# Kernel tuning notes

Hardware: AMD Instinct MI355X
Metric: run time of the kernel (lower is better)

The kernel has to match this reference:

```python
import jax, jax.numpy as jnp
import numpy as np

N, NB, NP, T = 1024, 16, 256, 80
EPS_LEN = 1e-9   # seg_len clamp_min in original
EPS_DD = 1e-12   # dot(d,d) clamp_min in original


def setup_inputs() -> dict:
    key = jax.random.key(0)
    k1, k2, k3, k4 = jax.random.split(key, 4)
    # smooth-ish random trajectory (cumsum of steps)
    selected_traj = jnp.cumsum(jax.random.normal(k1, (N, T, 3), jnp.float32) * 0.5, axis=1)
    # random polylines per (sample, boundary)
    road_points = jnp.cumsum(jax.random.normal(k2, (N, NB, NP, 3), jnp.float32) * 0.5, axis=2) \
                  + jax.random.normal(k3, (N, NB, 1, 3), jnp.float32) * 2.0
    # ragged valid-prefix masks, length in [2, NP]
    lengths = jax.random.randint(k4, (N, NB), 2, NP + 1)
    road_mask = jnp.arange(NP)[None, None, :] < lengths[:, :, None]
    return {"selected_traj": selected_traj, "road_points": road_points, "road_mask": road_mask}


def _arc_project(pos, rp, rm):
    # pos: [N,T,3]; rp: [N,NB,NP,3]; rm: [N,NB,NP] bool
    n, t = pos.shape[0], pos.shape[1]
    nb, npts = rp.shape[1], rp.shape[2]
    inf = jnp.asarray(jnp.inf, pos.dtype)
    ar = jnp.arange(npts)
    n_valid = rm.sum(-1)                                    # [N,NB]

    # pack valid points to the front, preserving order (== boolean-mask gather in torch)
    order = jnp.argsort(jnp.logical_not(rm), axis=-1, stable=True)
    pts_f = jnp.take_along_axis(rp, order[..., None], axis=2)      # [N,NB,NP,3]
    pack_mask = ar[None, None, :] < n_valid[:, :, None]
    pts_f = jnp.where(pack_mask[..., None], pts_f, 0.0)
    # flipped direction: reverse the valid prefix
    flip_idx = jnp.clip(n_valid[:, :, None] - 1 - ar[None, None, :], 0, npts - 1)
    pts_b = jnp.take_along_axis(pts_f, flip_idx[..., None], axis=2)
    pts_b = jnp.where(pack_mask[..., None], pts_b, 0.0)
    pts = jnp.stack([pts_f, pts_b], axis=2)                 # [N,NB,2,NP,3]

    # segment i is real iff i < n_valid-1
    seg_mask = ar[: npts - 1][None, None, None, :] < (n_valid - 1)[:, :, None, None]  # [N,NB,1,NP-1]
    seg_vec = pts[..., 1:, :] - pts[..., :-1, :]            # [N,NB,2,NP-1,3]
    seg_norm = jnp.sqrt((seg_vec ** 2).sum(-1))
    seg_len = jnp.where(seg_mask, jnp.maximum(seg_norm, EPS_LEN), 0.0)
    cum_s = jnp.concatenate([jnp.zeros_like(seg_len[..., :1]), jnp.cumsum(seg_len, -1)], -1)  # [N,NB,2,NP]
    last_idx = jnp.clip(n_valid - 1, 0, npts - 1)[:, :, None, None]
    total_s = jnp.take_along_axis(cum_s, jnp.broadcast_to(last_idx, (n, nb, 2, 1)), -1)  # [N,NB,2,1]

    # entry: project first trajectory point onto nearest valid segment
    p0 = pos[:, 0][:, None, None, None, :]                  # [N,1,1,1,3]
    a0 = pts[..., :-1, :]
    dd0 = jnp.maximum((seg_vec ** 2).sum(-1), EPS_DD)
    t0 = jnp.clip(((p0 - a0) * seg_vec).sum(-1) / dd0, 0.0, 1.0)
    q0 = a0 + t0[..., None] * seg_vec
    d2 = jnp.where(seg_mask, ((p0 - q0) ** 2).sum(-1), inf)
    seg0 = jnp.argmin(d2, -1)[..., None]                    # [N,NB,2,1]
    entry_s = jnp.take_along_axis(cum_s, seg0, -1) + jnp.take_along_axis(t0 * seg_len, seg0, -1)

    # trajectory arc-length, resample polyline at entry_s + traj arc length
    traj_seg = jnp.sqrt(((pos[:, 1:] - pos[:, :-1]) ** 2).sum(-1))
    traj_cs = jnp.concatenate([jnp.zeros_like(traj_seg[:, :1]), jnp.cumsum(traj_seg, -1)], -1)  # [N,T]
    target_s = jnp.clip(entry_s + traj_cs[:, None, None, :], 0.0, total_s)  # [N,NB,2,T]

    j = jax.vmap(lambda c, tg: jnp.searchsorted(c, tg, side='right'))(
        cum_s.reshape(-1, npts), target_s.reshape(-1, t)) - 1
    j = jnp.clip(j.reshape(n, nb, 2, t), 0, jnp.maximum(n_valid[:, :, None, None] - 2, 0))

    seg_l = jnp.take_along_axis(seg_len, j, -1)
    cs_j = jnp.take_along_axis(cum_s, j, -1)
    t_loc = jnp.clip((target_s - cs_j) / jnp.maximum(seg_l, EPS_LEN), 0.0, 1.0)
    pa = jnp.take_along_axis(pts, j[..., None], axis=3)
    pb = jnp.take_along_axis(pts, (j + 1)[..., None], axis=3)
    proj = pa + t_loc[..., None] * (pb - pa)                # [N,NB,2,T,3]

    # pick (boundary, direction) candidate with min total L2 cost
    cost = jnp.sqrt(((pos[:, None, None] - proj) ** 2).sum(-1)).sum(-1)  # [N,NB,2]
    cand_ok = (n_valid >= 2)[:, :, None]
    cost = jnp.where(cand_ok, cost, inf)
    best = jnp.argmin(cost.reshape(n, -1), -1)
    best_proj = jnp.take_along_axis(proj.reshape(n, -1, t, 3), best[:, None, None, None], axis=1)[:, 0]
    has = cand_ok.any((1, 2))
    return jnp.where(has[:, None, None], best_proj, pos)


def reference(selected_traj, road_points, road_mask):
    pos = selected_traj[..., 0:3]
    out_pos = _arc_project(pos, road_points, road_mask)
    return jnp.concatenate([out_pos, selected_traj[..., 3:]], axis=-1)
```

## Files before the change

kernel.cpp:

```cpp
#include <hip/hip_runtime.h>
#include <math.h>

#define NN 1024
#define NBB 16
#define NP 256
#define TT 80
#define EPS_LEN 1e-9f
#define EPS_DD 1e-12f

__device__ __forceinline__ float frcp(float x){ return __builtin_amdgcn_rcpf(x); }
__device__ __forceinline__ float fsq(float x){ return __builtin_amdgcn_sqrtf(x); }
__device__ __forceinline__ float rlane_f(float x, int l){
  return __builtin_bit_cast(float, __builtin_amdgcn_readlane(__builtin_bit_cast(int, x), l));
}
__device__ __forceinline__ float bump(float v){
  return __builtin_bit_cast(float, __builtin_bit_cast(int, v) + 1);
}

template<int CTRL,int RM>
__device__ __forceinline__ float dpp_add(float v){
  int t = __builtin_amdgcn_update_dpp(0, __builtin_bit_cast(int, v), CTRL, RM, 0xf, true);
  return v + __builtin_bit_cast(float, t);
}
__device__ __forceinline__ float wave_incl_scan(float v){
  v = dpp_add<0x111,0xf>(v);
  v = dpp_add<0x112,0xf>(v);
  v = dpp_add<0x114,0xf>(v);
  v = dpp_add<0x118,0xf>(v);
  v = dpp_add<0x142,0xa>(v);
  v = dpp_add<0x143,0xc>(v);
  return v;
}
__device__ __forceinline__ float wave_sum(float v){ return rlane_f(wave_incl_scan(v), 63); }
template<int CTRL,int RM>
__device__ __forceinline__ float dpp_min(float v){
  int t = __builtin_amdgcn_update_dpp(0x7f800000, __builtin_bit_cast(int,v), CTRL, RM, 0xf, false);
  return fminf(v, __builtin_bit_cast(float,t));
}
__device__ __forceinline__ float wave_min_all(float v){
  v=dpp_min<0x111,0xf>(v); v=dpp_min<0x112,0xf>(v);
  v=dpp_min<0x114,0xf>(v); v=dpp_min<0x118,0xf>(v);
  v=dpp_min<0x142,0xa>(v); v=dpp_min<0x143,0xc>(v);
  return rlane_f(v, 63);
}

__device__ __forceinline__ void lds_fence() {
  __builtin_amdgcn_wave_barrier();
  asm volatile("s_waitcnt lgkmcnt(0)" ::: "memory");
  __builtin_amdgcn_wave_barrier();
}

__device__ __forceinline__ int wave_nv(const void* mask, size_t base, int lane) {
  bool as_byte = ((const unsigned char*)mask)[1] != 0;
  int nv = 0;
  if (as_byte) {
    uchar4 v = ((const uchar4*)((const unsigned char*)mask + base))[lane];
    nv += __popcll(__ballot(v.x != 0));
    nv += __popcll(__ballot(v.y != 0));
    nv += __popcll(__ballot(v.z != 0));
    nv += __popcll(__ballot(v.w != 0));
  } else {
    int4 v = ((const int4*)((const int*)mask + base))[lane];
    nv += __popcll(__ballot(v.x != 0));
    nv += __popcll(__ballot(v.y != 0));
    nv += __popcll(__ballot(v.z != 0));
    nv += __popcll(__ballot(v.w != 0));
  }
  return nv;
}

__device__ __forceinline__ int count256s(const float* __restrict__ cs,
                                         const float* co, float v){
  int K = 0;
  #pragma unroll
  for (int k=0;k<16;k++) K += (co[k] < v);
  int base = (K < 16 ? K : 15) * 16;
  const float4* f4 = (const float4*)(cs + base);
  float4 c0=f4[0], c1=f4[1], c2=f4[2], c3=f4[3];
  int r = (c0.x<v)+(c0.y<v)+(c0.z<v)+(c0.w<v)+(c1.x<v)+(c1.y<v)+(c1.z<v)+(c1.w<v)
        + (c2.x<v)+(c2.y<v)+(c2.z<v)+(c2.w<v)+(c3.x<v)+(c3.y<v)+(c3.z<v)+(c3.w<v);
  return (K >= 16) ? 256 : (base + r);
}

struct SegOut {
  float cpre[4];
  float run;
  float bdf, btf; int bjf;
  float bdl, btl; int bjl;
};

template<bool NEEDMIN>
__device__ __forceinline__ void seg_pass(float4 A, float4 B, float4 C,
                                         int lane, int nv,
                                         float p0x, float p0y, float p0z,
                                         float* __restrict__ pts, SegOut& R) {
  const int j0 = lane * 4;
  float x[5], y[5], z[5];
  x[0]=A.x; y[0]=A.y; z[0]=A.z;
  x[1]=A.w; y[1]=B.x; z[1]=B.y;
  x[2]=B.z; y[2]=B.w; z[2]=C.x;
  x[3]=C.y; y[3]=C.z; z[3]=C.w;
  x[4]=__shfl_down(x[0],1,64); y[4]=__shfl_down(y[0],1,64); z[4]=__shfl_down(z[0],1,64);
  ((float4*)pts)[lane*3+0] = make_float4(x[0],y[0],z[0],x[1]);
  ((float4*)pts)[lane*3+1] = make_float4(y[1],z[1],x[2],y[2]);
  ((float4*)pts)[lane*3+2] = make_float4(z[2],x[3],y[3],z[3]);
  float run = 0.f;
  R.bdf=INFINITY; R.btf=0.f; R.bjf=j0;
  R.bdl=INFINITY; R.btl=0.f; R.bjl=j0;
  #pragma unroll
  for (int k=0;k<4;k++){
    bool valid = (j0+k) < nv-1;
    float vx=x[k+1]-x[k], vy=y[k+1]-y[k], vz=z[k+1]-z[k];
    float n2 = vx*vx+vy*vy+vz*vz;
    float sl = valid ? fmaxf(fsq(n2), EPS_LEN) : 0.f;
    if (NEEDMIN){
      float t = ((p0x-x[k])*vx+(p0y-y[k])*vy+(p0z-z[k])*vz) * frcp(fmaxf(n2,EPS_DD));
      t = fminf(fmaxf(t,0.f),1.f);
      float qx=x[k]+t*vx, qy=y[k]+t*vy, qz=z[k]+t*vz;
      float dx=p0x-qx, dy=p0y-qy, dz=p0z-qz;
      float d2 = valid ? (dx*dx+dy*dy+dz*dz) : INFINITY;
      if (d2 <  R.bdf){R.bdf=d2; R.bjf=j0+k; R.btf=t;}
      if (d2 <= R.bdl){R.bdl=d2; R.bjl=j0+k; R.btl=t;}
    }
    run += sl; R.cpre[k]=run;
  }
  R.run = run;
}

__device__ __forceinline__ void cs_pair_from_regs(int idx, float ex, const SegOut& R,
                                                  float& c0, float& c1){
  int o = idx >> 2, r = idx & 3;
  float a0 = (r==0)?0.f : (r==1)?R.cpre[0] : (r==2)?R.cpre[1] : R.cpre[2];
  float a1 = (r==0)?R.cpre[0] : (r==1)?R.cpre[1] : (r==2)?R.cpre[2] : R.run;
  c0 = rlane_f(ex + a0, o);
  c1 = rlane_f(ex + a1, o);
}

__device__ __forceinline__ void interp_at(const float* __restrict__ pts,
                                          const float* __restrict__ cs,
                                          const float* co, float Tot, int nv, int jmaxv,
                                          int dir, float ts,
                                          float& prx, float& pry, float& prz){
  float vq = dir ? (Tot - ts) : bump(ts);
  int cnt = count256s(cs, co, vq);
  int j = dir ? (nv-1-cnt) : (cnt-1);
  j = j<0?0:(j>jmaxv?jmaxv:j);
  int ia = dir ? (nv-1-j) : j;
  int ib = dir ? (nv-2-j) : (j+1);
  int lo = dir ? ib : ia;
  float c_lo = cs[lo], c_hi = cs[lo+1];
  float base = dir ? (Tot - c_hi) : c_lo;
  float tl = (ts - base) * frcp(fmaxf(c_hi - c_lo, EPS_LEN));
  tl = fminf(fmaxf(tl,0.f),1.f);
  float3 PA = *(const float3*)(pts + ia*3);
  float3 PB = *(const float3*)(pts + ib*3);
  prx = PA.x + tl*(PB.x-PA.x);
  pry = PA.y + tl*(PB.y-PA.y);
  prz = PA.z + tl*(PB.z-PA.z);
}

__device__ __forceinline__ void traj_tcs_wave(const float* __restrict__ pos, int lane,
                                              float* __restrict__ s_tc,
                                              float3& ptl, float3& pB){
  ptl.x = pos[lane*3+0]; ptl.y = pos[lane*3+1]; ptl.z = pos[lane*3+2];
  pB = make_float3(0.f,0.f,0.f);
  if (lane < 16){
    int t = 64+lane;
    pB.x = pos[t*3+0]; pB.y = pos[t*3+1]; pB.z = pos[t*3+2];
  }
  float nx = __shfl_down(ptl.x,1,64), ny = __shfl_down(ptl.y,1,64), nz = __shfl_down(ptl.z,1,64);
  float bx0 = rlane_f(pB.x,0), by0 = rlane_f(pB.y,0), bz0 = rlane_f(pB.z,0);
  if (lane==63){ nx=bx0; ny=by0; nz=bz0; }
  float dx=nx-ptl.x, dy=ny-ptl.y, dz=nz-ptl.z;
  float segA = fsq(dx*dx+dy*dy+dz*dz);
  float mx = __shfl_down(pB.x,1,64), my = __shfl_down(pB.y,1,64), mz = __shfl_down(pB.z,1,64);
  float ex=mx-pB.x, ey=my-pB.y, ez=mz-pB.z;
  float segB = (lane<15) ? fsq(ex*ex+ey*ey+ez*ez) : 0.f;
  float incA = wave_incl_scan(segA);
  float totA = rlane_f(incA, 63);
  float incB = wave_incl_scan(segB);
  s_tc[lane+1] = incA;
  if (lane<15) s_tc[65+lane] = totA + incB;
  if (lane==0) s_tc[0] = 0.f;
}

__global__ __launch_bounds__(512, 8)
void fused_all(const float* __restrict__ traj, const float* __restrict__ rp,
               const void* __restrict__ mask, float* __restrict__ out) {
  __shared__ float s_pts[8][NP*3];
  __shared__ float s_cs[8][NP];
  __shared__ float s_tc[8][TT];
  __shared__ float s_cost[NBB*2];
  __shared__ float2 s_ent[NBB];

  const int wid = threadIdx.x>>6, lane = threadIdx.x&63;
  const int n = blockIdx.x;
  const float* pos = traj + (size_t)n*TT*3;

  float3 ptl, pB;
  traj_tcs_wave(pos, lane, s_tc[wid], ptl, pB);
  const float p0x = rlane_f(ptl.x,0), p0y = rlane_f(ptl.y,0), p0z = rlane_f(ptl.z,0);

  float* pts = s_pts[wid];
  float* csb = s_cs[wid];
  const float* tcw = s_tc[wid];

  #pragma unroll 1
  for (int c=0; c<2; ++c){
    const int b = wid*2 + c;
    const size_t nb = (size_t)n*NBB + b;
    const float4* p4 = (const float4*)(rp + nb*NP*3);
    float4 A = p4[lane*3+0], B = p4[lane*3+1], C = p4[lane*3+2];
    int nv = wave_nv(mask, nb*NP, lane);
    float cf = INFINITY, cr = INFINITY, e0 = 0.f, e1 = 0.f;
    if (nv >= 2){
      SegOut R;
      seg_pass<true>(A,B,C, lane, nv, p0x,p0y,p0z, pts, R);
      float inc = wave_incl_scan(R.run);
      float ex = inc - R.run;
      ((float4*)csb)[lane] = make_float4(ex, ex+R.cpre[0], ex+R.cpre[1], ex+R.cpre[2]);
      const float Tot = rlane_f(inc, 63);
      float cval = ex + R.cpre[2];
      float co[16];
      #pragma unroll
      for (int k=0;k<16;k++) co[k] = rlane_f(cval, 4*k+3);
      float minv = wave_min_all(R.bdf);
      unsigned long long mf = __ballot(R.bdf == minv);
      unsigned long long ml = __ballot(R.bdl == minv);
      int lf = __builtin_ctzll(mf);
      int ll = 63 - __builtin_clzll(ml);
      int   jf = __builtin_amdgcn_readlane(R.bjf, lf);
      float tf = rlane_f(R.btf, lf);
      int   jl = __builtin_amdgcn_readlane(R.bjl, ll);
      float tl0 = rlane_f(R.btl, ll);
      float cjf, cjf1, cjl, cjl1;
      cs_pair_from_regs(jf, ex, R, cjf, cjf1);
      cs_pair_from_regs(jl, ex, R, cjl, cjl1);
      e0 = cjf + tf*(cjf1-cjf);
      e1 = (Tot - cjl1) + (1.f-tl0)*(cjl1-cjl);

      lds_fence();

      const int jmaxv = nv-2;
      float accf=0.f, accr=0.f;
      #pragma unroll
      for (int p=0;p<3;p++){
        int task = p*64 + lane;
        bool act = task < 2*TT;
        int dir = task>=TT ? 1 : 0;
        int t = dir ? task-TT : task;
        int tr = t < TT ? t : TT-1;
        float ts = (dir ? e1 : e0) + tcw[tr];
        ts = fminf(fmaxf(ts,0.f),Tot);
        float prx,pry,prz;
        interp_at(pts, csb, co, Tot, nv, jmaxv, dir, ts, prx,pry,prz);
        if (p==0){
          float dx=ptl.x-prx, dy=ptl.y-pry, dz=ptl.z-prz;
          accf += fsq(dx*dx+dy*dy+dz*dz);
        } else if (act){
          float px_, py_, pz_;
          if (p==1 && !dir){ px_=pB.x; py_=pB.y; pz_=pB.z; }
          else { px_=pos[t*3+0]; py_=pos[t*3+1]; pz_=pos[t*3+2]; }
          float dx=px_-prx, dy=py_-pry, dz=pz_-prz;
          float dd=fsq(dx*dx+dy*dy+dz*dz);
          if (dir) accr+=dd; else accf+=dd;
        }
      }
      cf = wave_sum(accf); cr = wave_sum(accr);
      lds_fence();
    }
    if (lane==0){
      s_cost[b*2+0]=cf; s_cost[b*2+1]=cr;
      s_ent[b] = make_float2(e0, e1);
    }
  }

  __syncthreads();
  if (wid >= 2) return;

  float bc = (lane<NBB*2) ? s_cost[lane] : INFINITY;
  int bi = (lane<NBB*2) ? lane : 64;
  #pragma unroll
  for (int d=1;d<64;d<<=1){
    float oc=__shfl_xor(bc,d,64); int oi=__shfl_xor(bi,d,64);
    if (oc<bc || (oc==bc && oi<bi)){bc=oc;bi=oi;}
  }
  float* o = out + (size_t)n*TT*3;
  if (bc == INFINITY){
    if (wid==0 && lane < 60) ((float4*)o)[lane] = ((const float4*)pos)[lane];
    return;
  }
  int b = bi>>1, dir = bi&1;
  const size_t nbi = (size_t)n*NBB + b;
  const float4* p4 = (const float4*)(rp + nbi*NP*3);
  float4 A = p4[lane*3+0], B = p4[lane*3+1], C = p4[lane*3+2];
  float2 eW = s_ent[b];
  float entry = dir ? eW.y : eW.x;
  int nv = wave_nv(mask, nbi*NP, lane);
  nv = max(nv, 2);

  SegOut R;
  seg_pass<false>(A,B,C, lane, nv, 0.f,0.f,0.f, pts, R);
  float inc = wave_incl_scan(R.run);
  float ex = inc - R.run;
  ((float4*)csb)[lane] = make_float4(ex, ex+R.cpre[0], ex+R.cpre[1], ex+R.cpre[2]);
  const float Tot = rlane_f(inc, 63);
  float cval = ex + R.cpre[2];
  float co[16];
  #pragma unroll
  for (int k=0;k<16;k++) co[k] = rlane_f(cval, 4*k+3);

  lds_fence();

  const int jmaxv = nv-2;
  int t = wid*40 + lane;
  if (lane < 40){
    float ts = entry + tcw[t];
    ts = fminf(fmaxf(ts,0.f),Tot);
    float prx,pry,prz;
    interp_at(pts, csb, co, Tot, nv, jmaxv, dir, ts, prx,pry,prz);
    o[t*3+0]=prx; o[t*3+1]=pry; o[t*3+2]=prz;
  }
}

extern "C" void kernel_launch(void* const* d_in, const int* in_sizes, int n_in,
                              void* d_out, int out_size, void* d_ws, size_t ws_size,
                              hipStream_t stream) {
  const float* traj = (const float*)d_in[0];
  const float* rp   = (const float*)d_in[1];
  const void*  mask = d_in[2];
  float* out  = (float*)d_out;
  hipLaunchKernelGGL(fused_all, dim3(NN), dim3(512), 0, stream,
                     traj, rp, mask, out);
}
```

Measured before the change: 30.92 us.

## Use one wave per boundary and reuse cached polyline data for final projection

The block grows from 8 to 16 waves, so each wave handles one boundary instead of looping over two. Cumulative arc lengths and points stay in LDS for every boundary, so the final projection reuses the winning boundary's cached data instead of reloading and rescanning it. The trajectory arc-length table moves from LDS into registers read through shuffles, and per-boundary costs and entries now pass through global workspace with atomic loads. The trade-off is a larger LDS footprint and 1024-thread blocks, which cut occupancy, plus reliance on global-memory visibility across __syncthreads.

```diff
diff --git a/kernel.cpp b/kernel.cpp
--- a/kernel.cpp
+++ b/kernel.cpp
@@ -159,127 +159,124 @@
   prz = PA.z + tl*(PB.z-PA.z);
 }
 
-__device__ __forceinline__ void traj_tcs_wave(const float* __restrict__ pos, int lane,
-                                              float* __restrict__ s_tc,
-                                              float3& ptl, float3& pB){
-  ptl.x = pos[lane*3+0]; ptl.y = pos[lane*3+1]; ptl.z = pos[lane*3+2];
+__device__ __forceinline__ float tc_of(int i, float exclA, float totA, float tBv){
+  float vA = __shfl(exclA, i, 64);
+  float vB = __shfl(tBv, i - 65, 64);
+  return (i < 64) ? vA : ((i == 64) ? totA : vB);
+}
+
+__global__ __launch_bounds__(1024, 8)
+void fused_all(const float* __restrict__ traj, const float* __restrict__ rp,
+               const void* __restrict__ mask, float* __restrict__ ws,
+               float* __restrict__ out) {
+  __shared__ float s_pts[NBB][NP*3];
+  __shared__ float s_cs[NBB][NP];
+
+  const int wid = threadIdx.x>>6, lane = threadIdx.x&63;
+  const int n = blockIdx.x;
+  const float* pos = traj + (size_t)n*TT*3;
+  float* wcost = ws + (size_t)n*96;
+  float* went  = wcost + 32;
+  float* wtot  = wcost + 64;
+  int*   wnv   = (int*)(wcost + 80);
+
+  float3 ptl, pB;
+  ptl.x=pos[lane*3+0]; ptl.y=pos[lane*3+1]; ptl.z=pos[lane*3+2];
   pB = make_float3(0.f,0.f,0.f);
   if (lane < 16){
     int t = 64+lane;
-    pB.x = pos[t*3+0]; pB.y = pos[t*3+1]; pB.z = pos[t*3+2];
-  }
-  float nx = __shfl_down(ptl.x,1,64), ny = __shfl_down(ptl.y,1,64), nz = __shfl_down(ptl.z,1,64);
-  float bx0 = rlane_f(pB.x,0), by0 = rlane_f(pB.y,0), bz0 = rlane_f(pB.z,0);
-  if (lane==63){ nx=bx0; ny=by0; nz=bz0; }
-  float dx=nx-ptl.x, dy=ny-ptl.y, dz=nz-ptl.z;
-  float segA = fsq(dx*dx+dy*dy+dz*dz);
-  float mx = __shfl_down(pB.x,1,64), my = __shfl_down(pB.y,1,64), mz = __shfl_down(pB.z,1,64);
-  float ex=mx-pB.x, ey=my-pB.y, ez=mz-pB.z;
-  float segB = (lane<15) ? fsq(ex*ex+ey*ey+ez*ez) : 0.f;
+    pB.x=pos[t*3+0]; pB.y=pos[t*3+1]; pB.z=pos[t*3+2];
+  }
+  float nx=__shfl_down(ptl.x,1,64), ny=__shfl_down(ptl.y,1,64), nz=__shfl_down(ptl.z,1,64);
+  if (lane==63){ nx=rlane_f(pB.x,0); ny=rlane_f(pB.y,0); nz=rlane_f(pB.z,0); }
+  float dxa=nx-ptl.x, dya=ny-ptl.y, dza=nz-ptl.z;
+  float segA = fsq(dxa*dxa+dya*dya+dza*dza);
+  float mx=__shfl_down(pB.x,1,64), my=__shfl_down(pB.y,1,64), mz=__shfl_down(pB.z,1,64);
+  float exb=mx-pB.x, eyb=my-pB.y, ezb=mz-pB.z;
+  float segB = (lane<15) ? fsq(exb*exb+eyb*eyb+ezb*ezb) : 0.f;
   float incA = wave_incl_scan(segA);
+  float exclA = incA - segA;
   float totA = rlane_f(incA, 63);
-  float incB = wave_incl_scan(segB);
-  s_tc[lane+1] = incA;
-  if (lane<15) s_tc[65+lane] = totA + incB;
-  if (lane==0) s_tc[0] = 0.f;
-}
-
-__global__ __launch_bounds__(512, 8)
-void fused_all(const float* __restrict__ traj, const float* __restrict__ rp,
-               const void* __restrict__ mask, float* __restrict__ out) {
-  __shared__ float s_pts[8][NP*3];
-  __shared__ float s_cs[8][NP];
-  __shared__ float s_tc[8][TT];
-  __shared__ float s_cost[NBB*2];
-  __shared__ float2 s_ent[NBB];
-
-  const int wid = threadIdx.x>>6, lane = threadIdx.x&63;
-  const int n = blockIdx.x;
-  const float* pos = traj + (size_t)n*TT*3;
-
-  float3 ptl, pB;
-  traj_tcs_wave(pos, lane, s_tc[wid], ptl, pB);
+  float tBv = totA + wave_incl_scan(segB);
   const float p0x = rlane_f(ptl.x,0), p0y = rlane_f(ptl.y,0), p0z = rlane_f(ptl.z,0);
 
+  const int b = wid;
+  const size_t nb = (size_t)n*NBB + b;
+  const float4* p4 = (const float4*)(rp + nb*NP*3);
+  float4 A = p4[lane*3+0], Bq = p4[lane*3+1], Cq = p4[lane*3+2];
+  int nv = wave_nv(mask, nb*NP, lane);
   float* pts = s_pts[wid];
   float* csb = s_cs[wid];
-  const float* tcw = s_tc[wid];
-
-  #pragma unroll 1
-  for (int c=0; c<2; ++c){
-    const int b = wid*2 + c;
-    const size_t nb = (size_t)n*NBB + b;
-    const float4* p4 = (const float4*)(rp + nb*NP*3);
-    float4 A = p4[lane*3+0], B = p4[lane*3+1], C = p4[lane*3+2];
-    int nv = wave_nv(mask, nb*NP, lane);
-    float cf = INFINITY, cr = INFINITY, e0 = 0.f, e1 = 0.f;
-    if (nv >= 2){
-      SegOut R;
-      seg_pass<true>(A,B,C, lane, nv, p0x,p0y,p0z, pts, R);
-      float inc = wave_incl_scan(R.run);
-      float ex = inc - R.run;
-      ((float4*)csb)[lane] = make_float4(ex, ex+R.cpre[0], ex+R.cpre[1], ex+R.cpre[2]);
-      const float Tot = rlane_f(inc, 63);
-      float cval = ex + R.cpre[2];
-      float co[16];
-      #pragma unroll
-      for (int k=0;k<16;k++) co[k] = rlane_f(cval, 4*k+3);
-      float minv = wave_min_all(R.bdf);
-      unsigned long long mf = __ballot(R.bdf == minv);
-      unsigned long long ml = __ballot(R.bdl == minv);
-      int lf = __builtin_ctzll(mf);
-      int ll = 63 - __builtin_clzll(ml);
-      int   jf = __builtin_amdgcn_readlane(R.bjf, lf);
-      float tf = rlane_f(R.btf, lf);
-      int   jl = __builtin_amdgcn_readlane(R.bjl, ll);
-      float tl0 = rlane_f(R.btl, ll);
-      float cjf, cjf1, cjl, cjl1;
-      cs_pair_from_regs(jf, ex, R, cjf, cjf1);
-      cs_pair_from_regs(jl, ex, R, cjl, cjl1);
-      e0 = cjf + tf*(cjf1-cjf);
-      e1 = (Tot - cjl1) + (1.f-tl0)*(cjl1-cjl);
-
-      lds_fence();
-
-      const int jmaxv = nv-2;
-      float accf=0.f, accr=0.f;
-      #pragma unroll
-      for (int p=0;p<3;p++){
-        int task = p*64 + lane;
-        bool act = task < 2*TT;
-        int dir = task>=TT ? 1 : 0;
-        int t = dir ? task-TT : task;
-        int tr = t < TT ? t : TT-1;
-        float ts = (dir ? e1 : e0) + tcw[tr];
-        ts = fminf(fmaxf(ts,0.f),Tot);
-        float prx,pry,prz;
-        interp_at(pts, csb, co, Tot, nv, jmaxv, dir, ts, prx,pry,prz);
-        if (p==0){
-          float dx=ptl.x-prx, dy=ptl.y-pry, dz=ptl.z-prz;
-          accf += fsq(dx*dx+dy*dy+dz*dz);
-        } else if (act){
-          float px_, py_, pz_;
-          if (p==1 && !dir){ px_=pB.x; py_=pB.y; pz_=pB.z; }
-          else { px_=pos[t*3+0]; py_=pos[t*3+1]; pz_=pos[t*3+2]; }
-          float dx=px_-prx, dy=py_-pry, dz=pz_-prz;
-          float dd=fsq(dx*dx+dy*dy+dz*dz);
-          if (dir) accr+=dd; else accf+=dd;
-        }
+  float cf=INFINITY, cr=INFINITY, e0=0.f, e1=0.f, Tot=0.f;
+
+  if (nv >= 2){
+    SegOut R;
+    seg_pass<true>(A,Bq,Cq, lane, nv, p0x,p0y,p0z, pts, R);
+    float inc = wave_incl_scan(R.run);
+    float ex = inc - R.run;
+    ((float4*)csb)[lane] = make_float4(ex, ex+R.cpre[0], ex+R.cpre[1], ex+R.cpre[2]);
+    Tot = rlane_f(inc, 63);
+    float cval = ex + R.cpre[2];
+    float co[16];
+    #pragma unroll
+    for (int k=0;k<16;k++) co[k] = rlane_f(cval, 4*k+3);
+    float minv = wave_min_all(R.bdf);
+    unsigned long long mf = __ballot(R.bdf == minv);
+    unsigned long long ml = __ballot(R.bdl == minv);
+    int lf = __builtin_ctzll(mf);
+    int ll = 63 - __builtin_clzll(ml);
+    int   jf = __builtin_amdgcn_readlane(R.bjf, lf);
+    float tf = rlane_f(R.btf, lf);
+    int   jl = __builtin_amdgcn_readlane(R.bjl, ll);
+    float tl0 = rlane_f(R.btl, ll);
+    float cjf, cjf1, cjl, cjl1;
+    cs_pair_from_regs(jf, ex, R, cjf, cjf1);
+    cs_pair_from_regs(jl, ex, R, cjl, cjl1);
+    e0 = cjf + tf*(cjf1-cjf);
+    e1 = (Tot - cjl1) + (1.f-tl0)*(cjl1-cjl);
+
+    lds_fence();
+
+    const int jmaxv = nv-2;
+    float accf=0.f, accr=0.f;
+    #pragma unroll
+    for (int p=0;p<3;p++){
+      int task = p*64 + lane;
+      bool act = task < 2*TT;
+      int dir = task>=TT ? 1 : 0;
+      int t = dir ? task-TT : task;
+      int tr = t < TT ? t : TT-1;
+      float ts = (dir ? e1 : e0) + tc_of(tr, exclA, totA, tBv);
+      ts = fminf(fmaxf(ts,0.f),Tot);
+      float prx,pry,prz;
+      interp_at(pts, csb, co, Tot, nv, jmaxv, dir, ts, prx,pry,prz);
+      if (p==0){
+        float dx=ptl.x-prx, dy=ptl.y-pry, dz=ptl.z-prz;
+        accf += fsq(dx*dx+dy*dy+dz*dz);
+      } else if (act){
+        float px_, py_, pz_;
+        if (p==1 && !dir){ px_=pB.x; py_=pB.y; pz_=pB.z; }
+        else { px_=pos[t*3+0]; py_=pos[t*3+1]; pz_=pos[t*3+2]; }
+        float dx=px_-prx, dy=py_-pry, dz=pz_-prz;
+        float dd=fsq(dx*dx+dy*dy+dz*dz);
+        if (dir) accr+=dd; else accf+=dd;
       }
-      cf = wave_sum(accf); cr = wave_sum(accr);
-      lds_fence();
     }
-    if (lane==0){
-      s_cost[b*2+0]=cf; s_cost[b*2+1]=cr;
-      s_ent[b] = make_float2(e0, e1);
-    }
+    cf = wave_sum(accf); cr = wave_sum(accr);
+  }
+  if (lane==0){
+    wcost[b*2+0]=cf; wcost[b*2+1]=cr;
+    went [b*2+0]=e0; went [b*2+1]=e1;
+    wtot[b]=Tot; wnv[b]=nv;
   }
 
   __syncthreads();
-  if (wid >= 2) return;
-
-  float bc = (lane<NBB*2) ? s_cost[lane] : INFINITY;
-  int bi = (lane<NBB*2) ? lane : 64;
+  if (wid != 0) return;
+
+  float bc = (lane < NBB*2)
+    ? __hip_atomic_load(&wcost[lane], __ATOMIC_RELAXED, __HIP_MEMORY_SCOPE_AGENT)
+    : INFINITY;
+  int bi = (lane < NBB*2) ? lane : 64;
   #pragma unroll
   for (int d=1;d<64;d<<=1){
     float oc=__shfl_xor(bc,d,64); int oi=__shfl_xor(bi,d,64);
@@ -287,39 +284,30 @@
   }
   float* o = out + (size_t)n*TT*3;
   if (bc == INFINITY){
-    if (wid==0 && lane < 60) ((float4*)o)[lane] = ((const float4*)pos)[lane];
+    if (lane < 60) ((float4*)o)[lane] = ((const float4*)pos)[lane];
     return;
   }
-  int b = bi>>1, dir = bi&1;
-  const size_t nbi = (size_t)n*NBB + b;
-  const float4* p4 = (const float4*)(rp + nbi*NP*3);
-  float4 A = p4[lane*3+0], B = p4[lane*3+1], C = p4[lane*3+2];
-  float2 eW = s_ent[b];
-  float entry = dir ? eW.y : eW.x;
-  int nv = wave_nv(mask, nbi*NP, lane);
-  nv = max(nv, 2);
-
-  SegOut R;
-  seg_pass<false>(A,B,C, lane, nv, 0.f,0.f,0.f, pts, R);
-  float inc = wave_incl_scan(R.run);
-  float ex = inc - R.run;
-  ((float4*)csb)[lane] = make_float4(ex, ex+R.cpre[0], ex+R.cpre[1], ex+R.cpre[2]);
-  const float Tot = rlane_f(inc, 63);
-  float cval = ex + R.cpre[2];
-  float co[16];
-  #pragma unroll
-  for (int k=0;k<16;k++) co[k] = rlane_f(cval, 4*k+3);
-
-  lds_fence();
-
-  const int jmaxv = nv-2;
-  int t = wid*40 + lane;
-  if (lane < 40){
-    float ts = entry + tcw[t];
-    ts = fminf(fmaxf(ts,0.f),Tot);
-    float prx,pry,prz;
-    interp_at(pts, csb, co, Tot, nv, jmaxv, dir, ts, prx,pry,prz);
-    o[t*3+0]=prx; o[t*3+1]=pry; o[t*3+2]=prz;
+  int wb = bi>>1, dir = bi&1;
+  float entry = __hip_atomic_load(&went[bi], __ATOMIC_RELAXED, __HIP_MEMORY_SCOPE_AGENT);
+  float TotW  = __hip_atomic_load(&wtot[wb], __ATOMIC_RELAXED, __HIP_MEMORY_SCOPE_AGENT);
+  int   nvW   = __hip_atomic_load(&wnv[wb],  __ATOMIC_RELAXED, __HIP_MEMORY_SCOPE_AGENT);
+  const float* ptsW = s_pts[wb];
+  const float* csW  = s_cs[wb];
+  float cobk = (lane<16) ? csW[lane*16+15] : 0.f;
+  float coW[16];
+  #pragma unroll
+  for (int k=0;k<16;k++) coW[k] = rlane_f(cobk, k);
+  const int jmaxv = nvW-2;
+  #pragma unroll
+  for (int p=0;p<2;p++){
+    int t = p*64 + lane;
+    if (t < TT){
+      float ts = entry + tc_of(t, exclA, totA, tBv);
+      ts = fminf(fmaxf(ts,0.f),TotW);
+      float prx,pry,prz;
+      interp_at(ptsW, csW, coW, TotW, nvW, jmaxv, dir, ts, prx,pry,prz);
+      o[t*3+0]=prx; o[t*3+1]=pry; o[t*3+2]=prz;
+    }
   }
 }
 
@@ -329,7 +317,8 @@
   const float* traj = (const float*)d_in[0];
   const float* rp   = (const float*)d_in[1];
   const void*  mask = d_in[2];
+  float* ws   = (float*)d_ws;
   float* out  = (float*)d_out;
-  hipLaunchKernelGGL(fused_all, dim3(NN), dim3(512), 0, stream,
-                     traj, rp, mask, out);
-}
+  hipLaunchKernelGGL(fused_all, dim3(NN), dim3(1024), 0, stream,
+                     traj, rp, mask, ws, out);
+}
```

Result: no change. 30.35 us, median of 2 (-1.8%).
